# Performance work log

Measured on AMD Instinct MI355X. Metric: run time of the kernel, lower is better.

Reference implementation:

```python
import jax, jax.numpy as jnp
import numpy as np

# Module hyperparameters (from init_kwargs)
THRESHOLD = 1.0
TAU_MEM = 20.0
TAU_ADP = 200.0
BETA = 0.1          # adaptive-threshold coupling
SG_BETA = 10.0      # fast_sigmoid surrogate slope
ALPHA_MEM = float(np.exp(-1.0 / TAU_MEM))
ALPHA_ADP = float(np.exp(-1.0 / TAU_ADP))


@jax.custom_vjp
def spike_fn(u):
    # SpikingFunction.forward: (input >= threshold).float()
    return (u >= THRESHOLD).astype(u.dtype)

def _spike_fwd(u):
    return spike_fn(u), u

def _spike_bwd(u, g):
    # fast_sigmoid surrogate on (input - threshold)
    return (g / (1.0 + jnp.abs(SG_BETA * (u - THRESHOLD))),)

spike_fn.defvjp(_spike_fwd, _spike_bwd)


def setup_inputs() -> dict:
    key = jax.random.key(0)
    x = jax.random.normal(key, (32, 512, 1024), dtype=jnp.float32)  # [B, T, D]
    return {"x": x}


def reference(x):
    B = x.shape[0]
    state_shape = (B,) + x.shape[2:]
    v0 = jnp.zeros(state_shape, dtype=x.dtype)  # membrane potential
    a0 = jnp.zeros(state_shape, dtype=x.dtype)  # adaptive threshold

    def step(carry, x_t):
        v, a = carry
        v = ALPHA_MEM * v + x_t
        cur_thr = THRESHOLD + BETA * a
        # NOTE: original passes (v - cur_thr) into a spike fn that itself
        # compares against THRESHOLD, so the threshold counts twice.
        s = spike_fn(v - cur_thr)
        a = ALPHA_ADP * a + s
        v = v - s * THRESHOLD  # reset == 'subtract'
        return (v, a), s

    x_tmajor = jnp.swapaxes(x, 0, 1)  # [T, B, D]
    _, spikes = jax.lax.scan(step, (v0, a0), x_tmajor)
    return jnp.swapaxes(spikes, 0, 1)  # [B, T, D]
```

## Files before the change

kernel.cpp:

```cpp
#include <hip/hip_runtime.h>


#define T_STEPS 512
#define D_DIM   1024
#define T_TILE  64
#define N_TILES (T_STEPS / T_TILE)
#define RING    3
#define LDS_PITCH 66

#define ALPHA_MEM 0.9512294245007141f
#define ALPHA_ADP 0.9950124791926823f

typedef float f32x4 __attribute__((ext_vector_type(4)));

__device__ __forceinline__ bool adlif_step(float xv, float& v, float& a) {
    v = __fadd_rn(__fmul_rn(ALPHA_MEM, v), xv);
    float cur = __fadd_rn(1.0f, __fmul_rn(0.1f, a));
    float u = __fsub_rn(v, cur);
    bool fired = (u >= 1.0f);
    float s = fired ? 1.0f : 0.0f;
    a = __fadd_rn(__fmul_rn(ALPHA_ADP, a), s);
    v = __fsub_rn(v, s);
    return fired;
}

__device__ __forceinline__ void load_tile(const float* __restrict__ xb, int t0,
                                          int lane, float (*buf)[LDS_PITCH]) {
    const int r0 = lane >> 4;
    const int m  = lane & 15;
    const float* src = xb + (size_t)(t0 + r0) * D_DIM + m * 4;
    f32x4 v[16];
#pragma unroll
    for (int i = 0; i < 16; ++i)
        v[i] = *reinterpret_cast<const f32x4*>(src + (size_t)i * 4 * D_DIM);
#pragma unroll
    for (int i = 0; i < 16; ++i)
        *reinterpret_cast<f32x4*>(&buf[i * 4 + r0][m * 4]) = v[i];
}

__global__ __launch_bounds__(512) void adlif_fused(const float* __restrict__ x,
                                                   float* __restrict__ out) {
    __shared__ float    tiles[RING][T_TILE][LDS_PITCH];
    __shared__ unsigned sbits[2][64][2];

    const int lane = threadIdx.x & 63;
    const int wave = threadIdx.x >> 6;
    const int bid  = blockIdx.x;
    const int b    = bid >> 4;
    const int dgrp = bid & 15;
    const float* xb = x   + (size_t)b * (T_STEPS * D_DIM) + dgrp * 64;
    float*       ob = out + (size_t)b * (T_STEPS * D_DIM) + dgrp * 64;

    if (wave == 1) load_tile(xb, 0 * T_TILE, lane, tiles[0]);
    if (wave == 2) load_tile(xb, 1 * T_TILE, lane, tiles[1]);
    __syncthreads();

    float v = 0.0f, a = 0.0f;

    for (int k = 0; k <= N_TILES; ++k) {
        if (wave == 0) {
            if (k < N_TILES) {
                unsigned wlo = 0u, whi = 0u;
#pragma unroll
                for (int j = 0; j < T_TILE; ++j) {
                    const float xv = tiles[k % RING][j][lane];
                    const bool f = adlif_step(xv, v, a);
                    if (j < 32) wlo |= ((unsigned)f) << j;
                    else        whi |= ((unsigned)f) << (j - 32);
                }
                sbits[k & 1][lane][0] = wlo;
                sbits[k & 1][lane][1] = whi;
            }
        } else if (wave <= 3) {
            const int t = k + 2;
            if (t < N_TILES && wave == (t % 3) + 1)
                load_tile(xb, t * T_TILE, lane, tiles[t % RING]);
        } else {
            if (k >= 1) {
                const int kt = k - 1;
                const int r0 = (wave - 4) * 16;
                const int c0 = (lane & 15) * 4;
                const int rl = lane >> 4;
                const int half = (r0 >= 32) ? 1 : 0;
                const unsigned w0 = sbits[kt & 1][c0 + 0][half];
                const unsigned w1 = sbits[kt & 1][c0 + 1][half];
                const unsigned w2 = sbits[kt & 1][c0 + 2][half];
                const unsigned w3 = sbits[kt & 1][c0 + 3][half];
#pragma unroll
                for (int i = 0; i < 4; ++i) {
                    const int r = r0 + i * 4 + rl;
                    const int bitpos = r & 31;
                    f32x4 val;
                    val.x = (float)((w0 >> bitpos) & 1u);
                    val.y = (float)((w1 >> bitpos) & 1u);
                    val.z = (float)((w2 >> bitpos) & 1u);
                    val.w = (float)((w3 >> bitpos) & 1u);
                    __builtin_nontemporal_store(
                        val, (f32x4*)(ob + (size_t)(kt * T_TILE + r) * D_DIM + c0));
                }
            }
        }
        __syncthreads();
    }
}

extern "C" void kernel_launch(void* const* d_in, const int* in_sizes, int n_in,
                              void* d_out, int out_size, void* d_ws, size_t ws_size,
                              hipStream_t stream) {
    const float* x = (const float*)d_in[0];
    float* out = (float*)d_out;

    const int total = in_sizes[0];
    const int channels = total / T_STEPS;
    const int blocks = channels / 64;

    adlif_fused<<<blocks, 512, 0, stream>>>(x, out);
}
```

Before: 26.08 us.

## Spread loads and stores across all waves with register-prefetched double buffering

Replaces the dedicated loader waves and three-slot LDS ring with a scheme where all eight waves each load two rows of the tile two steps ahead into registers and write them to a double-buffered LDS tile. All eight waves now also share the spike output stores. The block barrier is replaced by one that waits only on LDS counters, so the global loads held in registers can stay outstanding across iterations. This aims to hide global load latency behind the serial recurrence in wave 0, at the cost of relying on manual waitcnt handling for correctness.

Result: slower. 27.15 us (+4.1%).

```diff
diff --git a/kernel.cpp b/kernel.cpp
--- a/kernel.cpp
+++ b/kernel.cpp
@@ -5,7 +5,6 @@
 #define D_DIM   1024
 #define T_TILE  64
 #define N_TILES (T_STEPS / T_TILE)
-#define RING    3
 #define LDS_PITCH 66
 
 #define ALPHA_MEM 0.9512294245007141f
@@ -24,23 +23,16 @@
     return fired;
 }
 
-__device__ __forceinline__ void load_tile(const float* __restrict__ xb, int t0,
-                                          int lane, float (*buf)[LDS_PITCH]) {
-    const int r0 = lane >> 4;
-    const int m  = lane & 15;
-    const float* src = xb + (size_t)(t0 + r0) * D_DIM + m * 4;
-    f32x4 v[16];
-#pragma unroll
-    for (int i = 0; i < 16; ++i)
-        v[i] = *reinterpret_cast<const f32x4*>(src + (size_t)i * 4 * D_DIM);
-#pragma unroll
-    for (int i = 0; i < 16; ++i)
-        *reinterpret_cast<f32x4*>(&buf[i * 4 + r0][m * 4]) = v[i];
-}
+#define BARRIER_LGKM_ONLY() do {                                   \
+    asm volatile("s_waitcnt lgkmcnt(0)" ::: "memory");             \
+    __builtin_amdgcn_sched_barrier(0);                             \
+    __builtin_amdgcn_s_barrier();                                  \
+    __builtin_amdgcn_sched_barrier(0);                             \
+} while (0)
 
 __global__ __launch_bounds__(512) void adlif_fused(const float* __restrict__ x,
                                                    float* __restrict__ out) {
-    __shared__ float    tiles[RING][T_TILE][LDS_PITCH];
+    __shared__ float    tiles[2][T_TILE][LDS_PITCH];
     __shared__ unsigned sbits[2][64][2];
 
     const int lane = threadIdx.x & 63;
@@ -51,56 +43,74 @@
     const float* xb = x   + (size_t)b * (T_STEPS * D_DIM) + dgrp * 64;
     float*       ob = out + (size_t)b * (T_STEPS * D_DIM) + dgrp * 64;
 
-    if (wave == 1) load_tile(xb, 0 * T_TILE, lane, tiles[0]);
-    if (wave == 2) load_tile(xb, 1 * T_TILE, lane, tiles[1]);
-    __syncthreads();
+    const int rl = lane >> 4;
+    const int c0 = (lane & 15) * 4;
+    const int ra = wave * 8 + rl;
+    const int rb = wave * 8 + 4 + rl;
 
     float v = 0.0f, a = 0.0f;
 
+    f32x4 ld0 = *reinterpret_cast<const f32x4*>(xb + (size_t)(0 * T_TILE + ra) * D_DIM + c0);
+    f32x4 ld1 = *reinterpret_cast<const f32x4*>(xb + (size_t)(0 * T_TILE + rb) * D_DIM + c0);
+    f32x4 p0  = *reinterpret_cast<const f32x4*>(xb + (size_t)(1 * T_TILE + ra) * D_DIM + c0);
+    f32x4 p1  = *reinterpret_cast<const f32x4*>(xb + (size_t)(1 * T_TILE + rb) * D_DIM + c0);
+    *reinterpret_cast<f32x4*>(&tiles[0][ra][c0]) = ld0;
+    *reinterpret_cast<f32x4*>(&tiles[0][rb][c0]) = ld1;
+    ld0 = p0;
+    ld1 = p1;
+    BARRIER_LGKM_ONLY();
+
     for (int k = 0; k <= N_TILES; ++k) {
-        if (wave == 0) {
-            if (k < N_TILES) {
-                unsigned wlo = 0u, whi = 0u;
+        f32x4 nld0 = ld0, nld1 = ld1;
+        const int t2 = k + 2;
+        if (t2 < N_TILES) {
+            nld0 = *reinterpret_cast<const f32x4*>(xb + (size_t)(t2 * T_TILE + ra) * D_DIM + c0);
+            nld1 = *reinterpret_cast<const f32x4*>(xb + (size_t)(t2 * T_TILE + rb) * D_DIM + c0);
+        }
+
+        if (k + 1 < N_TILES) {
+            *reinterpret_cast<f32x4*>(&tiles[(k + 1) & 1][ra][c0]) = ld0;
+            *reinterpret_cast<f32x4*>(&tiles[(k + 1) & 1][rb][c0]) = ld1;
+        }
+
+        if (wave == 0 && k < N_TILES) {
+            unsigned wlo = 0u, whi = 0u;
 #pragma unroll
-                for (int j = 0; j < T_TILE; ++j) {
-                    const float xv = tiles[k % RING][j][lane];
-                    const bool f = adlif_step(xv, v, a);
-                    if (j < 32) wlo |= ((unsigned)f) << j;
-                    else        whi |= ((unsigned)f) << (j - 32);
-                }
-                sbits[k & 1][lane][0] = wlo;
-                sbits[k & 1][lane][1] = whi;
+            for (int j = 0; j < T_TILE; ++j) {
+                const float xv = tiles[k & 1][j][lane];
+                const bool f = adlif_step(xv, v, a);
+                if (j < 32) wlo |= ((unsigned)f) << j;
+                else        whi |= ((unsigned)f) << (j - 32);
             }
-        } else if (wave <= 3) {
-            const int t = k + 2;
-            if (t < N_TILES && wave == (t % 3) + 1)
-                load_tile(xb, t * T_TILE, lane, tiles[t % RING]);
-        } else {
-            if (k >= 1) {
-                const int kt = k - 1;
-                const int r0 = (wave - 4) * 16;
-                const int c0 = (lane & 15) * 4;
-                const int rl = lane >> 4;
-                const int half = (r0 >= 32) ? 1 : 0;
-                const unsigned w0 = sbits[kt & 1][c0 + 0][half];
-                const unsigned w1 = sbits[kt & 1][c0 + 1][half];
-                const unsigned w2 = sbits[kt & 1][c0 + 2][half];
-                const unsigned w3 = sbits[kt & 1][c0 + 3][half];
+            sbits[k & 1][lane][0] = wlo;
+            sbits[k & 1][lane][1] = whi;
+        }
+
+        if (k >= 1) {
+            const int kt = k - 1;
+            const int half = wave >> 2;
+            const unsigned w0 = sbits[kt & 1][c0 + 0][half];
+            const unsigned w1 = sbits[kt & 1][c0 + 1][half];
+            const unsigned w2 = sbits[kt & 1][c0 + 2][half];
+            const unsigned w3 = sbits[kt & 1][c0 + 3][half];
 #pragma unroll
-                for (int i = 0; i < 4; ++i) {
-                    const int r = r0 + i * 4 + rl;
-                    const int bitpos = r & 31;
-                    f32x4 val;
-                    val.x = (float)((w0 >> bitpos) & 1u);
-                    val.y = (float)((w1 >> bitpos) & 1u);
-                    val.z = (float)((w2 >> bitpos) & 1u);
-                    val.w = (float)((w3 >> bitpos) & 1u);
-                    __builtin_nontemporal_store(
-                        val, (f32x4*)(ob + (size_t)(kt * T_TILE + r) * D_DIM + c0));
-                }
+            for (int i = 0; i < 2; ++i) {
+                const int r      = wave * 8 + i * 4 + rl;
+                const int bitpos = (wave & 3) * 8 + i * 4 + rl;
+                f32x4 val;
+                val.x = (float)((w0 >> bitpos) & 1u);
+                val.y = (float)((w1 >> bitpos) & 1u);
+                val.z = (float)((w2 >> bitpos) & 1u);
+                val.w = (float)((w3 >> bitpos) & 1u);
+                __builtin_nontemporal_store(
+                    val, (f32x4*)(ob + (size_t)(kt * T_TILE + r) * D_DIM + c0));
             }
         }
-        __syncthreads();
+
+        ld0 = nld0;
+        ld1 = nld1;
+
+        BARRIER_LGKM_ONLY();
     }
 }
 
```
